# Optimization experiments

Hardware: AMD Instinct MI355X
Metric: run time of the kernel (lower is better)

The kernel has to match this reference:

```python
import jax, jax.numpy as jnp
import numpy as np

N_NODES = 100000
N_EDGES = 3200000
N_GRAPHS = 4096
IN_CH = 128
HID = 128


def setup_inputs() -> dict:
    key = jax.random.key(0)
    ks = jax.random.split(key, 16)
    x = jax.random.normal(ks[0], (N_NODES, IN_CH), dtype=jnp.float32)
    edge_index = jax.random.randint(ks[1], (2, N_EDGES), 0, N_NODES, dtype=jnp.int64)
    batch = jnp.sort(jax.random.randint(ks[2], (N_NODES,), 0, N_GRAPHS, dtype=jnp.int64))
    def lin(k, fan_in, fan_out):
        bound = 1.0 / np.sqrt(fan_in)
        kw, kb = jax.random.split(k)
        W = jax.random.uniform(kw, (fan_in, fan_out), minval=-bound, maxval=bound, dtype=jnp.float32)
        b = jax.random.uniform(kb, (fan_out,), minval=-bound, maxval=bound, dtype=jnp.float32)
        return W, b
    W1, b1 = lin(ks[3], IN_CH, HID)
    W2, b2 = lin(ks[4], HID, HID)
    W3, b3 = lin(ks[5], HID, HID)
    lw1, lb1 = lin(ks[6], HID, HID // 2)
    lw2, lb2 = lin(ks[7], HID // 2, 1)
    return {"x": x, "edge_index": edge_index, "batch": batch,
            "W1": W1, "b1": b1, "W2": W2, "b2": b2, "W3": W3, "b3": b3,
            "lw1": lw1, "lb1": lb1, "lw2": lw2, "lb2": lb2}


def _gcn_conv(x, src, dst, norm, W, b, n_nodes):
    h = x @ W                              # [N, out]
    msg = h[src] * norm[:, None]           # gather + scale  [E+N, out]
    agg = jax.ops.segment_sum(msg, dst, num_segments=n_nodes)  # scatter-add
    return agg + b


def reference(x, edge_index, batch, W1, b1, W2, b2, W3, b3, lw1, lb1, lw2, lb2):
    n = x.shape[0]
    loop = jnp.arange(n, dtype=edge_index.dtype)
    src = jnp.concatenate([edge_index[0], loop])   # self-loops appended
    dst = jnp.concatenate([edge_index[1], loop])
    deg = jax.ops.segment_sum(jnp.ones_like(dst, dtype=x.dtype), dst, num_segments=n)
    dinv = deg ** -0.5                              # deg >= 1 due to self-loops
    norm = dinv[src] * dinv[dst]                    # symmetric normalization

    h = x
    for W, b in ((W1, b1), (W2, b2), (W3, b3)):
        h = jax.nn.relu(_gcn_conv(h, src, dst, norm, W, b, n))
        # dropout is identity in eval mode

    # global mean pool over graphs
    sums = jax.ops.segment_sum(h, batch, num_segments=N_GRAPHS)
    counts = jax.ops.segment_sum(jnp.ones((n,), dtype=h.dtype), batch, num_segments=N_GRAPHS)
    pooled = sums / jnp.maximum(counts, 1.0)[:, None]   # [G, HID]

    out = jax.nn.relu(pooled @ lw1 + lb1)
    out = out @ lw2 + lb2
    return out[:, 0]
```

## Files before the change

### kernel.cpp

```cpp
#include <hip/hip_runtime.h>


constexpr int HID = 128;
constexpr int BIN_SHIFT = 8;
constexpr int MAXBINS = 512;

static __device__ __forceinline__ void fma4(float4& a, float s, const float4& b) {
    a.x += s * b.x; a.y += s * b.y; a.z += s * b.z; a.w += s * b.w;
}
static __device__ __forceinline__ unsigned bf16rne(float f) {
    unsigned u = __float_as_uint(f);
    return (u + 0x7FFFu + ((u >> 16) & 1u)) >> 16;
}
static __device__ __forceinline__ unsigned packbf16(float lo, float hi) {
    return bf16rne(lo) | (bf16rne(hi) << 16);
}
static __device__ __forceinline__ float blo(unsigned u) { return __uint_as_float(u << 16); }
static __device__ __forceinline__ float bhi(unsigned u) { return __uint_as_float(u & 0xFFFF0000u); }

__global__ __launch_bounds__(256) void k_binhist(const int* __restrict__ dst,
                                                 int* __restrict__ binc,
                                                 int nE, int nbins) {
    __shared__ int h[MAXBINS];
    const int tid = threadIdx.x;
    for (int t = tid; t < nbins; t += 256) h[t] = 0;
    __syncthreads();
    const long long e0 = (long long)blockIdx.x * 4096;
#pragma unroll
    for (int k = 0; k < 16; ++k) {
        long long e = e0 + k * 256 + tid;
        if (e < nE) atomicAdd(&h[dst[e] >> BIN_SHIFT], 1);
    }
    __syncthreads();
    for (int t = tid; t < nbins; t += 256)
        if (h[t]) atomicAdd(&binc[t], h[t]);
}

__global__ __launch_bounds__(512) void k_scanbins(const int* __restrict__ binc,
                                                  int* __restrict__ bin_start,
                                                  int* __restrict__ bin_cursor,
                                                  int nbins, int nE) {
    __shared__ int lds[512];
    const int tid = threadIdx.x;
    int v = (tid < nbins) ? binc[tid] : 0;
    lds[tid] = v;
    __syncthreads();
    for (int off = 1; off < 512; off <<= 1) {
        int u = (tid >= off) ? lds[tid - off] : 0;
        __syncthreads();
        lds[tid] += u;
        __syncthreads();
    }
    int excl = lds[tid] - v;
    if (tid < nbins) { bin_start[tid] = excl; bin_cursor[tid] = excl; }
    if (tid == 0) bin_start[nbins] = nE;
}

__global__ __launch_bounds__(256) void k_stage(const int* __restrict__ src,
                                               const int* __restrict__ dst,
                                               int* __restrict__ bin_cursor,
                                               int2* __restrict__ staged,
                                               int nE, int nbins) {
    __shared__ int hist[MAXBINS];
    __shared__ int wbase[MAXBINS];
    __shared__ int rank[MAXBINS];
    const int tid = threadIdx.x;
    const long long e0 = (long long)blockIdx.x * 4096;
    int es[16], ed[16];
#pragma unroll
    for (int k = 0; k < 16; ++k) {
        long long e = e0 + k * 256 + tid;
        if (e < nE) { es[k] = src[e]; ed[k] = dst[e]; }
        else        { es[k] = 0; ed[k] = -1; }
    }
    for (int t = tid; t < nbins; t += 256) { hist[t] = 0; rank[t] = 0; }
    __syncthreads();
#pragma unroll
    for (int k = 0; k < 16; ++k)
        if (ed[k] >= 0) atomicAdd(&hist[ed[k] >> BIN_SHIFT], 1);
    __syncthreads();
    for (int t = tid; t < nbins; t += 256)
        wbase[t] = hist[t] ? atomicAdd(&bin_cursor[t], hist[t]) : 0;
    __syncthreads();
#pragma unroll
    for (int k = 0; k < 16; ++k)
        if (ed[k] >= 0) {
            int b = ed[k] >> BIN_SHIFT;
            int r = atomicAdd(&rank[b], 1);
            staged[wbase[b] + r] = make_int2(es[k], ed[k]);
        }
}

__global__ __launch_bounds__(256) void k_place2(const int* __restrict__ bin_start,
                                                const int2* __restrict__ staged,
                                                int* __restrict__ esrc,
                                                int* __restrict__ row_start,
                                                float* __restrict__ dinv, int nN) {
    __shared__ int cnt[1 << BIN_SHIFT];
    __shared__ int sc[1 << BIN_SHIFT];
    const int b = blockIdx.x;
    const int tid = threadIdx.x;
    const int d0 = b << BIN_SHIFT;
    const int dend = min(d0 + (1 << BIN_SHIFT), nN);
    const int p0 = bin_start[b];
    const int p1 = bin_start[b + 1];
    cnt[tid] = 0;
    __syncthreads();
    for (int i = p0 + tid; i < p1; i += 256)
        atomicAdd(&cnt[staged[i].y - d0], 1);
    __syncthreads();
    const int my = cnt[tid];
    sc[tid] = my;
    __syncthreads();
    for (int off = 1; off < 256; off <<= 1) {
        int v = (tid >= off) ? sc[tid - off] : 0;
        __syncthreads();
        sc[tid] += v;
        __syncthreads();
    }
    const int excl = sc[tid] - my;
    const int d = d0 + tid;
    if (d < dend) {
        row_start[d] = p0 + excl;
        dinv[d] = rsqrtf((float)my + 1.0f);
    }
    if (tid == 0 && dend == nN) row_start[nN] = p1;
    __syncthreads();
    cnt[tid] = p0 + excl;
    __syncthreads();
    for (int i = p0 + tid; i < p1; i += 256) {
        int2 pr = staged[i];
        int pos = atomicAdd(&cnt[pr.y - d0], 1);
        esrc[pos] = pr.x;
    }
}

__global__ __launch_bounds__(256) void k_gemm3(const float* __restrict__ A,
                                               const float* __restrict__ W,
                                               const float* __restrict__ dinv,
                                               unsigned* __restrict__ h16, int n) {
    __shared__ float As[64][68];
    __shared__ float Ws[64][128];
    const int tid = threadIdx.x;
    const int tc = tid & 15;
    const int tr = tid >> 4;
    const int row0 = blockIdx.x * 64;

    float4 acc0[4] = {}, acc1[4] = {};

    for (int pass = 0; pass < 2; ++pass) {
        const int kb = pass * 64;
        for (int it = 0; it < 4; ++it) {
            int flat = it * 256 + tid;
            int r = flat >> 4, k4 = flat & 15;
            int gr = row0 + r;
            float4 v = make_float4(0.f, 0.f, 0.f, 0.f);
            if (gr < n) v = *(const float4*)(A + (size_t)gr * HID + kb + k4 * 4);
            *(float4*)(&As[r][k4 * 4]) = v;
        }
        for (int it = 0; it < 8; ++it) {
            int flat = it * 256 + tid;
            int k = flat >> 5, c4 = flat & 31;
            *(float4*)(&Ws[k][c4 * 4]) = *(const float4*)(W + (size_t)(kb + k) * HID + c4 * 4);
        }
        __syncthreads();

#pragma unroll 2
        for (int k4 = 0; k4 < 16; ++k4) {
            float ar[4][4];
            *(float4*)&ar[0][0] = *(const float4*)(&As[tr * 4 + 0][k4 * 4]);
            *(float4*)&ar[1][0] = *(const float4*)(&As[tr * 4 + 1][k4 * 4]);
            *(float4*)&ar[2][0] = *(const float4*)(&As[tr * 4 + 2][k4 * 4]);
            *(float4*)&ar[3][0] = *(const float4*)(&As[tr * 4 + 3][k4 * 4]);
#pragma unroll
            for (int j = 0; j < 4; ++j) {
                float4 b0 = *(const float4*)(&Ws[k4 * 4 + j][tc * 4]);
                float4 b1 = *(const float4*)(&Ws[k4 * 4 + j][64 + tc * 4]);
#pragma unroll
                for (int i = 0; i < 4; ++i) {
                    fma4(acc0[i], ar[i][j], b0);
                    fma4(acc1[i], ar[i][j], b1);
                }
            }
        }
        __syncthreads();
    }

#pragma unroll
    for (int i = 0; i < 4; ++i) {
        int r = row0 + tr * 4 + i;
        if (r < n) {
            float di = dinv[r];
            float4 a0 = acc0[i], a1 = acc1[i];
            uint2 p0, p1;
            p0.x = packbf16(a0.x * di, a0.y * di);
            p0.y = packbf16(a0.z * di, a0.w * di);
            p1.x = packbf16(a1.x * di, a1.y * di);
            p1.y = packbf16(a1.z * di, a1.w * di);
            *(uint2*)(h16 + (size_t)r * 64 + tc * 2) = p0;
            *(uint2*)(h16 + (size_t)r * 64 + 32 + tc * 2) = p1;
        }
    }
}

__global__ __launch_bounds__(256) void k_gemm3b(const unsigned* __restrict__ A16,
                                                const float* __restrict__ W,
                                                const float* __restrict__ dinv,
                                                unsigned* __restrict__ h16, int n) {
    __shared__ float As[64][68];
    __shared__ float Ws[64][128];
    const int tid = threadIdx.x;
    const int tc = tid & 15;
    const int tr = tid >> 4;
    const int row0 = blockIdx.x * 64;

    float4 acc0[4] = {}, acc1[4] = {};

    for (int pass = 0; pass < 2; ++pass) {
        const int kb = pass * 64;
        for (int it = 0; it < 4; ++it) {
            int flat = it * 256 + tid;
            int r = flat >> 4, q = flat & 15;
            int gr = row0 + r;
            uint2 u = make_uint2(0u, 0u);
            if (gr < n) u = *(const uint2*)(A16 + (size_t)gr * 64 + kb / 2 + q * 2);
            float4 w = make_float4(blo(u.x), bhi(u.x), blo(u.y), bhi(u.y));
            *(float4*)(&As[r][q * 4]) = w;
        }
        for (int it = 0; it < 8; ++it) {
            int flat = it * 256 + tid;
            int k = flat >> 5, c4 = flat & 31;
            *(float4*)(&Ws[k][c4 * 4]) = *(const float4*)(W + (size_t)(kb + k) * HID + c4 * 4);
        }
        __syncthreads();

#pragma unroll 2
        for (int k4 = 0; k4 < 16; ++k4) {
            float ar[4][4];
            *(float4*)&ar[0][0] = *(const float4*)(&As[tr * 4 + 0][k4 * 4]);
            *(float4*)&ar[1][0] = *(const float4*)(&As[tr * 4 + 1][k4 * 4]);
            *(float4*)&ar[2][0] = *(const float4*)(&As[tr * 4 + 2][k4 * 4]);
            *(float4*)&ar[3][0] = *(const float4*)(&As[tr * 4 + 3][k4 * 4]);
#pragma unroll
            for (int j = 0; j < 4; ++j) {
                float4 b0 = *(const float4*)(&Ws[k4 * 4 + j][tc * 4]);
                float4 b1 = *(const float4*)(&Ws[k4 * 4 + j][64 + tc * 4]);
#pragma unroll
                for (int i = 0; i < 4; ++i) {
                    fma4(acc0[i], ar[i][j], b0);
                    fma4(acc1[i], ar[i][j], b1);
                }
            }
        }
        __syncthreads();
    }

#pragma unroll
    for (int i = 0; i < 4; ++i) {
        int r = row0 + tr * 4 + i;
        if (r < n) {
            float di = dinv[r];
            float4 a0 = acc0[i], a1 = acc1[i];
            uint2 p0, p1;
            p0.x = packbf16(a0.x * di, a0.y * di);
            p0.y = packbf16(a0.z * di, a0.w * di);
            p1.x = packbf16(a1.x * di, a1.y * di);
            p1.y = packbf16(a1.z * di, a1.w * di);
            *(uint2*)(h16 + (size_t)r * 64 + tc * 2) = p0;
            *(uint2*)(h16 + (size_t)r * 64 + 32 + tc * 2) = p1;
        }
    }
}

__global__ __launch_bounds__(256) void k_agg16(const int* __restrict__ row_start,
                                               const int* __restrict__ esrc,
                                               const float* __restrict__ dinv,
                                               const unsigned* __restrict__ h16,
                                               const float* __restrict__ bias,
                                               unsigned* __restrict__ out16, int n,
                                               float* __restrict__ pool_sums,
                                               const int* __restrict__ batch) {
    int t = blockIdx.x * 256 + threadIdx.x;
    int node = t >> 6;
    if (node >= n) return;
    const int lane = t & 63;
    int e0 = row_start[node], e1 = row_start[node + 1];
    e0 = __builtin_amdgcn_readfirstlane(e0);
    e1 = __builtin_amdgcn_readfirstlane(e1);
    float dd = dinv[node];

    unsigned su = h16[(size_t)node * 64 + lane];
    float ax = blo(su), ay = bhi(su);

    int e = e0;
    for (; e + 4 <= e1; e += 4) {
        int s0 = __builtin_amdgcn_readfirstlane(esrc[e + 0]);
        int s1 = __builtin_amdgcn_readfirstlane(esrc[e + 1]);
        int s2 = __builtin_amdgcn_readfirstlane(esrc[e + 2]);
        int s3 = __builtin_amdgcn_readfirstlane(esrc[e + 3]);
        unsigned u0 = h16[(size_t)s0 * 64 + lane];
        unsigned u1 = h16[(size_t)s1 * 64 + lane];
        unsigned u2 = h16[(size_t)s2 * 64 + lane];
        unsigned u3 = h16[(size_t)s3 * 64 + lane];
        ax += blo(u0) + blo(u1) + blo(u2) + blo(u3);
        ay += bhi(u0) + bhi(u1) + bhi(u2) + bhi(u3);
    }
    for (; e < e1; ++e) {
        int s = __builtin_amdgcn_readfirstlane(esrc[e]);
        unsigned u = h16[(size_t)s * 64 + lane];
        ax += blo(u);
        ay += bhi(u);
    }

    const float2 bv = *(const float2*)(bias + 2 * lane);
    float ox = fmaxf(ax * dd + bv.x, 0.f);
    float oy = fmaxf(ay * dd + bv.y, 0.f);
    if (out16) {
        out16[(size_t)node * 64 + lane] = packbf16(ox, oy);
    } else {
        float* p = &pool_sums[(size_t)batch[node] * HID + 2 * lane];
        atomicAdd(p, ox);
        atomicAdd(p + 1, oy);
    }
}

__global__ __launch_bounds__(256) void k_count(const int* __restrict__ batch,
                                               float* __restrict__ cnt, int n) {
    int i = blockIdx.x * 256 + threadIdx.x;
    if (i < n) atomicAdd(&cnt[batch[i]], 1.0f);
}

__global__ __launch_bounds__(64) void k_mlp(const float* __restrict__ sums,
                                            const float* __restrict__ cnt,
                                            const float* __restrict__ lw1,
                                            const float* __restrict__ lb1,
                                            const float* __restrict__ lw2,
                                            const float* __restrict__ lb2,
                                            float* __restrict__ out) {
    int g = blockIdx.x;
    int j = threadIdx.x;
    float inv = 1.0f / fmaxf(cnt[g], 1.0f);
    const float* srow = sums + (size_t)g * HID;
    float acc = lb1[j];
#pragma unroll 8
    for (int k = 0; k < HID; ++k) acc += srow[k] * inv * lw1[k * 64 + j];
    acc = fmaxf(acc, 0.0f);
    float prod = acc * lw2[j];
#pragma unroll
    for (int off = 32; off > 0; off >>= 1) prod += __shfl_down(prod, off);
    if (j == 0) out[g] = prod + lb2[0];
}

extern "C" void kernel_launch(void* const* d_in, const int* in_sizes, int n_in,
                              void* d_out, int out_size, void* d_ws, size_t ws_size,
                              hipStream_t stream) {
    const float* x   = (const float*)d_in[0];
    const int*   ei  = (const int*)d_in[1];
    const int*   bat = (const int*)d_in[2];
    const float* W1  = (const float*)d_in[3];
    const float* b1  = (const float*)d_in[4];
    const float* W2  = (const float*)d_in[5];
    const float* b2  = (const float*)d_in[6];
    const float* W3  = (const float*)d_in[7];
    const float* b3  = (const float*)d_in[8];
    const float* lw1 = (const float*)d_in[9];
    const float* lb1 = (const float*)d_in[10];
    const float* lw2 = (const float*)d_in[11];
    const float* lb2 = (const float*)d_in[12];
    float* out = (float*)d_out;

    const int nN = in_sizes[2];
    const int nE = in_sizes[1] / 2;
    const int G  = out_size;
    const int* src = ei;
    const int* dst = ei + nE;

    const int nbins = (nN + (1 << BIN_SHIFT) - 1) >> BIN_SHIFT;

    char* p = (char*)d_ws;
    auto alloc = [&](size_t bytes) { char* r = p; p += (bytes + 255) & ~(size_t)255; return r; };
    unsigned* act16     = (unsigned*)alloc(sizeof(unsigned) * (size_t)nN * 64);
    unsigned* h16       = (unsigned*)alloc(sizeof(unsigned) * (size_t)nN * 64);
    float*    dinv      = (float*)alloc(sizeof(float) * nN);
    float*    sums      = (float*)alloc(sizeof(float) * (size_t)G * HID);
    float*    cnt       = (float*)alloc(sizeof(float) * G);
    int*      binc      = (int*)alloc(sizeof(int) * (nbins + 1));
    int*      bin_start = (int*)alloc(sizeof(int) * (nbins + 1));
    int*      bin_cur   = (int*)alloc(sizeof(int) * (nbins + 1));
    int*      row_start = (int*)alloc(sizeof(int) * (nN + 1));
    int*      esrc      = (int*)alloc(sizeof(int) * (size_t)nE);
    int2*     staged    = (int2*)h16;

    const int gemmGrid = (nN + 63) / 64;
    const int aggGrid  = (int)(((long long)nN * 64 + 255) / 256);
    const int edgeWGs  = (int)(((long long)nE + 4095) / 4096);

    hipMemsetAsync(binc, 0, sizeof(int) * nbins, stream);
    k_binhist<<<edgeWGs, 256, 0, stream>>>(dst, binc, nE, nbins);
    k_scanbins<<<1, 512, 0, stream>>>(binc, bin_start, bin_cur, nbins, nE);
    k_stage<<<edgeWGs, 256, 0, stream>>>(src, dst, bin_cur, staged, nE, nbins);
    k_place2<<<nbins, 256, 0, stream>>>(bin_start, staged, esrc, row_start, dinv, nN);

    hipMemsetAsync(sums, 0, sizeof(float) * ((size_t)G * HID + G), stream);
    k_count<<<(nN + 255) / 256, 256, 0, stream>>>(bat, cnt, nN);

    k_gemm3 <<<gemmGrid, 256, 0, stream>>>(x, W1, dinv, h16, nN);
    k_agg16 <<<aggGrid, 256, 0, stream>>>(row_start, esrc, dinv, h16, b1, act16, nN, nullptr, nullptr);
    k_gemm3b<<<gemmGrid, 256, 0, stream>>>(act16, W2, dinv, h16, nN);
    k_agg16 <<<aggGrid, 256, 0, stream>>>(row_start, esrc, dinv, h16, b2, act16, nN, nullptr, nullptr);
    k_gemm3b<<<gemmGrid, 256, 0, stream>>>(act16, W3, dinv, h16, nN);
    k_agg16 <<<aggGrid, 256, 0, stream>>>(row_start, esrc, dinv, h16, b3, nullptr, nN, sums, bat);

    k_mlp<<<G, 64, 0, stream>>>(sums, cnt, lw1, lb1, lw2, lb2, out);
}
```

Measured before the change: 635.8 us.

## Replace FP32 SIMT node GEMMs with bf16 MFMA matrix-core kernel

Replaces the two FP32 shared-memory register-tiled GEMM kernels with a single templated kernel using the 16x16x32 bf16 MFMA instruction. Weights are packed to bf16 in LDS in transposed layout, and activations are loaded directly into registers (x is converted to bf16 on load). Results are staged through LDS and then scaled by dinv and packed to bf16. This cuts the GEMM compute cost, at the price of bf16 rounding on the x input and on the weights.

```diff
diff --git a/kernel.cpp b/kernel.cpp
--- a/kernel.cpp
+++ b/kernel.cpp
@@ -5,9 +5,9 @@
 constexpr int BIN_SHIFT = 8;
 constexpr int MAXBINS = 512;
 
-static __device__ __forceinline__ void fma4(float4& a, float s, const float4& b) {
-    a.x += s * b.x; a.y += s * b.y; a.z += s * b.z; a.w += s * b.w;
-}
+typedef float f32x4 __attribute__((ext_vector_type(4)));
+typedef short short8 __attribute__((ext_vector_type(8)));
+
 static __device__ __forceinline__ unsigned bf16rne(float f) {
     unsigned u = __float_as_uint(f);
     return (u + 0x7FFFu + ((u >> 16) & 1u)) >> 16;
@@ -135,139 +135,80 @@
     }
 }
 
-__global__ __launch_bounds__(256) void k_gemm3(const float* __restrict__ A,
-                                               const float* __restrict__ W,
-                                               const float* __restrict__ dinv,
-                                               unsigned* __restrict__ h16, int n) {
-    __shared__ float As[64][68];
-    __shared__ float Ws[64][128];
-    const int tid = threadIdx.x;
-    const int tc = tid & 15;
-    const int tr = tid >> 4;
+template <bool A_F32>
+__global__ __launch_bounds__(256) void k_gemm_mfma(const void* __restrict__ Aptr,
+                                                   const float* __restrict__ W,
+                                                   const float* __restrict__ dinv,
+                                                   unsigned* __restrict__ h16, int n) {
+    __shared__ unsigned lds[128 * 68];
+    const int tid  = threadIdx.x;
+    const int lane = tid & 63;
+    const int w    = tid >> 6;
+    const int colb = lane & 15;
+    const int kg   = lane >> 4;
     const int row0 = blockIdx.x * 64;
 
-    float4 acc0[4] = {}, acc1[4] = {};
-
-    for (int pass = 0; pass < 2; ++pass) {
-        const int kb = pass * 64;
-        for (int it = 0; it < 4; ++it) {
-            int flat = it * 256 + tid;
-            int r = flat >> 4, k4 = flat & 15;
-            int gr = row0 + r;
-            float4 v = make_float4(0.f, 0.f, 0.f, 0.f);
-            if (gr < n) v = *(const float4*)(A + (size_t)gr * HID + kb + k4 * 4);
-            *(float4*)(&As[r][k4 * 4]) = v;
+    for (int it = 0; it < 32; ++it) {
+        int f = it * 256 + tid;
+        int c = f & 127, k2 = f >> 7;
+        float w0 = W[(size_t)(2 * k2) * HID + c];
+        float w1 = W[(size_t)(2 * k2 + 1) * HID + c];
+        lds[c * 68 + k2] = packbf16(w0, w1);
+    }
+
+    const int r = row0 + w * 16 + colb;
+    uint4 a[4] = {};
+    if (r < n) {
+        if constexpr (A_F32) {
+            const float* A = (const float*)Aptr;
+#pragma unroll
+            for (int kc = 0; kc < 4; ++kc) {
+                const float* p = A + (size_t)r * HID + kc * 32 + kg * 8;
+                float4 f0 = *(const float4*)(p);
+                float4 f1 = *(const float4*)(p + 4);
+                a[kc].x = packbf16(f0.x, f0.y);
+                a[kc].y = packbf16(f0.z, f0.w);
+                a[kc].z = packbf16(f1.x, f1.y);
+                a[kc].w = packbf16(f1.z, f1.w);
+            }
+        } else {
+            const unsigned* A16 = (const unsigned*)Aptr;
+#pragma unroll
+            for (int kc = 0; kc < 4; ++kc)
+                a[kc] = *(const uint4*)(A16 + (size_t)r * 64 + kc * 16 + kg * 4);
         }
-        for (int it = 0; it < 8; ++it) {
-            int flat = it * 256 + tid;
-            int k = flat >> 5, c4 = flat & 31;
-            *(float4*)(&Ws[k][c4 * 4]) = *(const float4*)(W + (size_t)(kb + k) * HID + c4 * 4);
+    }
+    __syncthreads();
+
+    f32x4 acc[8] = {};
+#pragma unroll
+    for (int ct = 0; ct < 8; ++ct) {
+#pragma unroll
+        for (int kc = 0; kc < 4; ++kc) {
+            uint4 bu = *(const uint4*)&lds[(ct * 16 + colb) * 68 + kc * 16 + kg * 4];
+            acc[ct] = __builtin_amdgcn_mfma_f32_16x16x32_bf16(
+                __builtin_bit_cast(short8, a[kc]),
+                __builtin_bit_cast(short8, bu),
+                acc[ct], 0, 0, 0);
         }
-        __syncthreads();
-
-#pragma unroll 2
-        for (int k4 = 0; k4 < 16; ++k4) {
-            float ar[4][4];
-            *(float4*)&ar[0][0] = *(const float4*)(&As[tr * 4 + 0][k4 * 4]);
-            *(float4*)&ar[1][0] = *(const float4*)(&As[tr * 4 + 1][k4 * 4]);
-            *(float4*)&ar[2][0] = *(const float4*)(&As[tr * 4 + 2][k4 * 4]);
-            *(float4*)&ar[3][0] = *(const float4*)(&As[tr * 4 + 3][k4 * 4]);
-#pragma unroll
-            for (int j = 0; j < 4; ++j) {
-                float4 b0 = *(const float4*)(&Ws[k4 * 4 + j][tc * 4]);
-                float4 b1 = *(const float4*)(&Ws[k4 * 4 + j][64 + tc * 4]);
-#pragma unroll
-                for (int i = 0; i < 4; ++i) {
-                    fma4(acc0[i], ar[i][j], b0);
-                    fma4(acc1[i], ar[i][j], b1);
-                }
-            }
-        }
-        __syncthreads();
-    }
-
-#pragma unroll
-    for (int i = 0; i < 4; ++i) {
-        int r = row0 + tr * 4 + i;
-        if (r < n) {
-            float di = dinv[r];
-            float4 a0 = acc0[i], a1 = acc1[i];
-            uint2 p0, p1;
-            p0.x = packbf16(a0.x * di, a0.y * di);
-            p0.y = packbf16(a0.z * di, a0.w * di);
-            p1.x = packbf16(a1.x * di, a1.y * di);
-            p1.y = packbf16(a1.z * di, a1.w * di);
-            *(uint2*)(h16 + (size_t)r * 64 + tc * 2) = p0;
-            *(uint2*)(h16 + (size_t)r * 64 + 32 + tc * 2) = p1;
-        }
-    }
-}
-
-__global__ __launch_bounds__(256) void k_gemm3b(const unsigned* __restrict__ A16,
-                                                const float* __restrict__ W,
-                                                const float* __restrict__ dinv,
-                                                unsigned* __restrict__ h16, int n) {
-    __shared__ float As[64][68];
-    __shared__ float Ws[64][128];
-    const int tid = threadIdx.x;
-    const int tc = tid & 15;
-    const int tr = tid >> 4;
-    const int row0 = blockIdx.x * 64;
-
-    float4 acc0[4] = {}, acc1[4] = {};
-
-    for (int pass = 0; pass < 2; ++pass) {
-        const int kb = pass * 64;
-        for (int it = 0; it < 4; ++it) {
-            int flat = it * 256 + tid;
-            int r = flat >> 4, q = flat & 15;
-            int gr = row0 + r;
-            uint2 u = make_uint2(0u, 0u);
-            if (gr < n) u = *(const uint2*)(A16 + (size_t)gr * 64 + kb / 2 + q * 2);
-            float4 w = make_float4(blo(u.x), bhi(u.x), blo(u.y), bhi(u.y));
-            *(float4*)(&As[r][q * 4]) = w;
-        }
-        for (int it = 0; it < 8; ++it) {
-            int flat = it * 256 + tid;
-            int k = flat >> 5, c4 = flat & 31;
-            *(float4*)(&Ws[k][c4 * 4]) = *(const float4*)(W + (size_t)(kb + k) * HID + c4 * 4);
-        }
-        __syncthreads();
-
-#pragma unroll 2
-        for (int k4 = 0; k4 < 16; ++k4) {
-            float ar[4][4];
-            *(float4*)&ar[0][0] = *(const float4*)(&As[tr * 4 + 0][k4 * 4]);
-            *(float4*)&ar[1][0] = *(const float4*)(&As[tr * 4 + 1][k4 * 4]);
-            *(float4*)&ar[2][0] = *(const float4*)(&As[tr * 4 + 2][k4 * 4]);
-            *(float4*)&ar[3][0] = *(const float4*)(&As[tr * 4 + 3][k4 * 4]);
-#pragma unroll
-            for (int j = 0; j < 4; ++j) {
-                float4 b0 = *(const float4*)(&Ws[k4 * 4 + j][tc * 4]);
-                float4 b1 = *(const float4*)(&Ws[k4 * 4 + j][64 + tc * 4]);
-#pragma unroll
-                for (int i = 0; i < 4; ++i) {
-                    fma4(acc0[i], ar[i][j], b0);
-                    fma4(acc1[i], ar[i][j], b1);
-                }
-            }
-        }
-        __syncthreads();
-    }
-
-#pragma unroll
-    for (int i = 0; i < 4; ++i) {
-        int r = row0 + tr * 4 + i;
-        if (r < n) {
-            float di = dinv[r];
-            float4 a0 = acc0[i], a1 = acc1[i];
-            uint2 p0, p1;
-            p0.x = packbf16(a0.x * di, a0.y * di);
-            p0.y = packbf16(a0.z * di, a0.w * di);
-            p1.x = packbf16(a1.x * di, a1.y * di);
-            p1.y = packbf16(a1.z * di, a1.w * di);
-            *(uint2*)(h16 + (size_t)r * 64 + tc * 2) = p0;
-            *(uint2*)(h16 + (size_t)r * 64 + 32 + tc * 2) = p1;
+    }
+
+    __syncthreads();
+    float* Cb = (float*)lds;
+#pragma unroll
+    for (int ct = 0; ct < 8; ++ct)
+#pragma unroll
+        for (int reg = 0; reg < 4; ++reg)
+            Cb[(w * 16 + kg * 4 + reg) * 132 + ct * 16 + colb] = acc[ct][reg];
+    __syncthreads();
+    for (int it = 0; it < 16; ++it) {
+        int f = it * 256 + tid;
+        int rl = f >> 6, cw = f & 63;
+        int gr = row0 + rl;
+        if (gr < n) {
+            float di = dinv[gr];
+            float2 v = *(const float2*)&Cb[rl * 132 + 2 * cw];
+            h16[(size_t)gr * 64 + cw] = packbf16(v.x * di, v.y * di);
         }
     }
 }
@@ -404,12 +345,12 @@
     hipMemsetAsync(sums, 0, sizeof(float) * ((size_t)G * HID + G), stream);
     k_count<<<(nN + 255) / 256, 256, 0, stream>>>(bat, cnt, nN);
 
-    k_gemm3 <<<gemmGrid, 256, 0, stream>>>(x, W1, dinv, h16, nN);
-    k_agg16 <<<aggGrid, 256, 0, stream>>>(row_start, esrc, dinv, h16, b1, act16, nN, nullptr, nullptr);
-    k_gemm3b<<<gemmGrid, 256, 0, stream>>>(act16, W2, dinv, h16, nN);
-    k_agg16 <<<aggGrid, 256, 0, stream>>>(row_start, esrc, dinv, h16, b2, act16, nN, nullptr, nullptr);
-    k_gemm3b<<<gemmGrid, 256, 0, stream>>>(act16, W3, dinv, h16, nN);
-    k_agg16 <<<aggGrid, 256, 0, stream>>>(row_start, esrc, dinv, h16, b3, nullptr, nN, sums, bat);
+    k_gemm_mfma<true ><<<gemmGrid, 256, 0, stream>>>(x, W1, dinv, h16, nN);
+    k_agg16<<<aggGrid, 256, 0, stream>>>(row_start, esrc, dinv, h16, b1, act16, nN, nullptr, nullptr);
+    k_gemm_mfma<false><<<gemmGrid, 256, 0, stream>>>(act16, W2, dinv, h16, nN);
+    k_agg16<<<aggGrid, 256, 0, stream>>>(row_start, esrc, dinv, h16, b2, act16, nN, nullptr, nullptr);
+    k_gemm_mfma<false><<<gemmGrid, 256, 0, stream>>>(act16, W3, dinv, h16, nN);
+    k_agg16<<<aggGrid, 256, 0, stream>>>(row_start, esrc, dinv, h16, b3, nullptr, nN, sums, bat);
 
     k_mlp<<<G, 64, 0, stream>>>(sums, cnt, lw1, lb1, lw2, lb2, out);
 }
```

Measured after the change: 533.0 us. 1.19x faster.
